# Optimization experiments

Measured on AMD Instinct MI355X. Metric: run time of the kernel, lower is better.

## Reference

```python
import jax, jax.numpy as jnp
import numpy as np

NUM_ENTS = 1000
NUM_RELS = 100
HIDDEN = 200
N_QUERY = 50000
N_HIST = 1000000
ALPHA = 0.5


def setup_inputs() -> dict:
    key = jax.random.key(0)
    ks = jax.random.split(key, 12)
    s = 0.05  # small init for numerical stability (xavier-like scale)
    return {
        "ent_emb": jax.random.normal(ks[0], (NUM_ENTS, HIDDEN), jnp.float32) * s,
        "rel_emb": jax.random.normal(ks[1], (NUM_RELS, HIDDEN), jnp.float32) * s,
        "tim_emb": jax.random.normal(ks[2], (1, HIDDEN), jnp.float32) * s,
        "g_w": jax.random.normal(ks[3], (3 * HIDDEN, HIDDEN), jnp.float32) * s,
        "g_b": jnp.zeros((HIDDEN,), jnp.float32),
        "c_w": jax.random.normal(ks[4], (3 * HIDDEN, HIDDEN), jnp.float32) * s,
        "c_b": jnp.zeros((HIDDEN,), jnp.float32),
        "hist_sub": jax.random.randint(ks[5], (N_HIST,), 0, NUM_ENTS, jnp.int32),
        "hist_rel": jax.random.randint(ks[6], (N_HIST,), 0, NUM_RELS, jnp.int32),
        "hist_obj": jax.random.randint(ks[7], (N_HIST,), 0, NUM_ENTS, jnp.int32),
        "sub": jax.random.randint(ks[8], (N_QUERY,), 0, NUM_ENTS, jnp.int32),
        "rel": jax.random.randint(ks[9], (N_QUERY,), 0, NUM_RELS, jnp.int32),
    }


def reference(ent_emb, rel_emb, tim_emb, g_w, g_b, c_w, c_b,
              hist_sub, hist_rel, hist_obj, sub, rel):
    E = ent_emb.shape[0]
    R = rel_emb.shape[0]
    N = sub.shape[0]
    # Triple-count histogram over all history graphs (fused scatter-add;
    # equivalent to the per-graph python loop vocab[s,r,o] += 1).
    vocab = jnp.zeros((E, R, E), jnp.float32).at[hist_sub, hist_rel, hist_obj].add(1.0)
    # Query features: [N, 3H]
    x = jnp.concatenate(
        [ent_emb[sub], rel_emb[rel], jnp.broadcast_to(tim_emb, (N, tim_emb.shape[1]))],
        axis=1)
    # Generate-mode score distribution
    gscore = jax.nn.softmax(x @ g_w + g_b, axis=1)  # [N, H]
    # Copy-mode mask: 1 where the (sub, rel) pair occurred in history
    mask = (vocab[sub, rel].sum(axis=1, keepdims=True) != 0).astype(x.dtype)  # [N, 1]
    cscore = jax.nn.softmax(jnp.tanh(x @ c_w + c_b) + mask, axis=1)  # [N, H]
    fscore = gscore + ALPHA * (cscore - gscore)
    return jnp.log(fscore)
```

## Files before the change

kernel.cpp:

```cpp
#include <hip/hip_runtime.h>
#include <math.h>

#define HIDDEN 200
#define LOG2E 1.4426950408889634f
#define LN2   0.6931471805599453f

typedef float f32x4 __attribute__((ext_vector_type(4)));

__global__ __launch_bounds__(256) void precompute_kernel(
    const float* __restrict__ ent, const float* __restrict__ rel,
    const float* __restrict__ tim,
    const float* __restrict__ g_w, const float* __restrict__ g_b,
    const float* __restrict__ c_w, const float* __restrict__ c_b,
    float* __restrict__ EA, float* __restrict__ EB) {
  const int mode = blockIdx.y;
  const float* w = mode ? c_w : g_w;
  const float* bias = mode ? c_b : g_b;
  const bool is_ent = blockIdx.x < 500;
  const int row0 = is_ent ? blockIdx.x * 2 : (blockIdx.x - 500) * 2;
  const float* in = is_ent ? ent : rel;
  const int k0 = is_ent ? 0 : 200;
  float* obase = is_ent ? (EA + row0 * 400 + mode * 200)
                        : (EB + row0 * 400 + mode * 200);

  __shared__ float a0[HIDDEN], a1[HIDDEN], tl[HIDDEN];
  const int c = threadIdx.x;
  if (c < HIDDEN) {
    a0[c] = in[row0 * HIDDEN + c];
    a1[c] = in[(row0 + 1) * HIDDEN + c];
    if (!is_ent) tl[c] = tim[c];
  }
  __syncthreads();
  if (c >= HIDDEN) return;

  const float* wp = w + k0 * HIDDEN + c;
  float acc0a = 0.f, acc0b = 0.f, acc1a = 0.f, acc1b = 0.f;
  #pragma unroll 4
  for (int k = 0; k < 100; ++k) {
    float w0 = wp[k * HIDDEN];
    float w1 = wp[(k + 100) * HIDDEN];
    acc0a += a0[k] * w0;
    acc0b += a0[k + 100] * w1;
    acc1a += a1[k] * w0;
    acc1b += a1[k + 100] * w1;
  }
  float r0 = acc0a + acc0b;
  float r1 = acc1a + acc1b;
  if (!is_ent) {
    const float* wt = w + 400 * HIDDEN + c;
    float ta = 0.f, tb = 0.f;
    #pragma unroll 4
    for (int k = 0; k < 100; ++k) {
      ta += tl[k] * wt[k * HIDDEN];
      tb += tl[k + 100] * wt[(k + 100) * HIDDEN];
    }
    float extra = ta + tb + bias[c];
    r0 += extra;
    r1 += extra;
  }
  if (mode == 0) {
    r0 = __builtin_amdgcn_exp2f(r0 * LOG2E);
    r1 = __builtin_amdgcn_exp2f(r1 * LOG2E);
  }
  obase[c] = r0;
  obase[400 + c] = r1;
}

__global__ __launch_bounds__(256) void query_kernel(
    const float* __restrict__ EA, const float* __restrict__ EB,
    const int* __restrict__ sub, const int* __restrict__ rel,
    float* __restrict__ out, int N) {
  int gtid = blockIdx.x * blockDim.x + threadIdx.x;
  int q = gtid >> 6;
  int lane = threadIdx.x & 63;
  if (q >= N) return;

  int s = __builtin_amdgcn_readfirstlane(sub[q]);
  int r = __builtin_amdgcn_readfirstlane(rel[q]);
  bool act = lane < (HIDDEN / 4);

  const f32x4* ea = (const f32x4*)(EA + s * 400);
  const f32x4* eb = (const f32x4*)(EB + r * 400);

  f32x4 eg, ec;
  float sg = 0.f, sc = 0.f;
  if (act) {
    eg = ea[lane] * eb[lane];
    sg = (eg[0] + eg[1]) + (eg[2] + eg[3]);
    f32x4 xc = ea[lane + 50] + eb[lane + 50];
    #pragma unroll
    for (int j = 0; j < 4; ++j) {
      float e2 = __builtin_amdgcn_exp2f(xc[j] * (2.f * LOG2E));
      float th = (e2 - 1.f) * __builtin_amdgcn_rcpf(e2 + 1.f);
      ec[j] = __builtin_amdgcn_exp2f(th * LOG2E);
      sc += ec[j];
    }
  }
  #pragma unroll
  for (int m = 32; m > 0; m >>= 1) {
    sg += __shfl_xor(sg, m);
    sc += __shfl_xor(sc, m);
  }

  if (act) {
    float kl = __builtin_amdgcn_logf(2.f * sg * sc) * LN2;
    f32x4 o;
    #pragma unroll
    for (int j = 0; j < 4; ++j) {
      float num = eg[j] * sc + ec[j] * sg;
      o[j] = fmaf(__builtin_amdgcn_logf(num), LN2, -kl);
    }
    __builtin_nontemporal_store(o, (f32x4*)(out + q * HIDDEN) + lane);
  }
}

extern "C" void kernel_launch(void* const* d_in, const int* in_sizes, int n_in,
                              void* d_out, int out_size, void* d_ws, size_t ws_size,
                              hipStream_t stream) {
  const float* ent  = (const float*)d_in[0];
  const float* relE = (const float*)d_in[1];
  const float* tim  = (const float*)d_in[2];
  const float* g_w  = (const float*)d_in[3];
  const float* g_b  = (const float*)d_in[4];
  const float* c_w  = (const float*)d_in[5];
  const float* c_b  = (const float*)d_in[6];
  const int* sub = (const int*)d_in[10];
  const int* rel = (const int*)d_in[11];
  float* out = (float*)d_out;
  int N = in_sizes[10];

  float* ws = (float*)d_ws;
  float* EA = ws;
  float* EB = ws + 400000;

  dim3 grid1(550, 2);
  precompute_kernel<<<grid1, 256, 0, stream>>>(ent, relE, tim, g_w, g_b, c_w,
                                               c_b, EA, EB);

  long long threads = (long long)N * 64;
  int blocks = (int)((threads + 255) / 256);
  query_kernel<<<blocks, 256, 0, stream>>>(EA, EB, sub, rel, out, N);
}
```

Before: 125.2 us.

## Precompute per (sub,rel) softmax normalizers and drop wave reductions in query kernel

Adds a pair_kernel that computes the gen and copy softmax denominators for all 1000x100 (sub,rel) pairs into workspace tables. The query kernel then reads these sums and maps one thread per float4 output, so it no longer needs a 64-lane wavefront per query, idle lanes, or shuffle reductions. The cost is an extra launch and a sequential 200-step loop per pair, which computes 100k pairs against 50k queries, plus a gather into the SG/SC tables.

New measurement: 141.8 us. 13.2% more time.

```diff
diff --git a/kernel.cpp b/kernel.cpp
--- a/kernel.cpp
+++ b/kernel.cpp
@@ -66,52 +66,61 @@
   obase[400 + c] = r1;
 }
 
+__global__ __launch_bounds__(128) void pair_kernel(
+    const float* __restrict__ EA, const float* __restrict__ EB,
+    float* __restrict__ SG, float* __restrict__ SC) {
+  const int s = blockIdx.x;
+  __shared__ float row[400];
+  for (int i = threadIdx.x; i < 400; i += 128) row[i] = EA[s * 400 + i];
+  __syncthreads();
+  const int r = threadIdx.x;
+  if (r >= 100) return;
+
+  const float* ebg = EB + r * 400;
+  const float* ebc = ebg + 200;
+  float sg = 0.f, sc = 0.f;
+  #pragma unroll 4
+  for (int k = 0; k < 200; ++k) {
+    sg = fmaf(row[k], ebg[k], sg);
+    float x = row[200 + k] + ebc[k];
+    float e2 = __builtin_amdgcn_exp2f(x * (2.f * LOG2E));
+    float th = (e2 - 1.f) * __builtin_amdgcn_rcpf(e2 + 1.f);
+    sc += __builtin_amdgcn_exp2f(th * LOG2E);
+  }
+  SG[s * 100 + r] = sg;
+  SC[s * 100 + r] = sc;
+}
+
 __global__ __launch_bounds__(256) void query_kernel(
     const float* __restrict__ EA, const float* __restrict__ EB,
+    const float* __restrict__ SG, const float* __restrict__ SC,
     const int* __restrict__ sub, const int* __restrict__ rel,
-    float* __restrict__ out, int N) {
-  int gtid = blockIdx.x * blockDim.x + threadIdx.x;
-  int q = gtid >> 6;
-  int lane = threadIdx.x & 63;
-  if (q >= N) return;
+    float* __restrict__ out, int total) {
+  int t = blockIdx.x * blockDim.x + threadIdx.x;
+  if (t >= total) return;
+  unsigned q = (unsigned)t / 50u;
+  unsigned j = (unsigned)t - q * 50u;
 
-  int s = __builtin_amdgcn_readfirstlane(sub[q]);
-  int r = __builtin_amdgcn_readfirstlane(rel[q]);
-  bool act = lane < (HIDDEN / 4);
+  int s = sub[q];
+  int r = rel[q];
+  float isg = 0.5f * __builtin_amdgcn_rcpf(SG[s * 100 + r]);
+  float isc = 0.5f * __builtin_amdgcn_rcpf(SC[s * 100 + r]);
 
   const f32x4* ea = (const f32x4*)(EA + s * 400);
   const f32x4* eb = (const f32x4*)(EB + r * 400);
+  f32x4 eg = ea[j] * eb[j];
+  f32x4 xc = ea[j + 50] + eb[j + 50];
 
-  f32x4 eg, ec;
-  float sg = 0.f, sc = 0.f;
-  if (act) {
-    eg = ea[lane] * eb[lane];
-    sg = (eg[0] + eg[1]) + (eg[2] + eg[3]);
-    f32x4 xc = ea[lane + 50] + eb[lane + 50];
-    #pragma unroll
-    for (int j = 0; j < 4; ++j) {
-      float e2 = __builtin_amdgcn_exp2f(xc[j] * (2.f * LOG2E));
-      float th = (e2 - 1.f) * __builtin_amdgcn_rcpf(e2 + 1.f);
-      ec[j] = __builtin_amdgcn_exp2f(th * LOG2E);
-      sc += ec[j];
-    }
+  f32x4 o;
+  #pragma unroll
+  for (int i = 0; i < 4; ++i) {
+    float e2 = __builtin_amdgcn_exp2f(xc[i] * (2.f * LOG2E));
+    float th = (e2 - 1.f) * __builtin_amdgcn_rcpf(e2 + 1.f);
+    float ec = __builtin_amdgcn_exp2f(th * LOG2E);
+    float v = fmaf(eg[i], isg, ec * isc);
+    o[i] = __builtin_amdgcn_logf(v) * LN2;
   }
-  #pragma unroll
-  for (int m = 32; m > 0; m >>= 1) {
-    sg += __shfl_xor(sg, m);
-    sc += __shfl_xor(sc, m);
-  }
-
-  if (act) {
-    float kl = __builtin_amdgcn_logf(2.f * sg * sc) * LN2;
-    f32x4 o;
-    #pragma unroll
-    for (int j = 0; j < 4; ++j) {
-      float num = eg[j] * sc + ec[j] * sg;
-      o[j] = fmaf(__builtin_amdgcn_logf(num), LN2, -kl);
-    }
-    __builtin_nontemporal_store(o, (f32x4*)(out + q * HIDDEN) + lane);
-  }
+  __builtin_nontemporal_store(o, (f32x4*)out + t);
 }
 
 extern "C" void kernel_launch(void* const* d_in, const int* in_sizes, int n_in,
@@ -132,12 +141,16 @@
   float* ws = (float*)d_ws;
   float* EA = ws;
   float* EB = ws + 400000;
+  float* SG = ws + 440000;
+  float* SC = ws + 540000;
 
   dim3 grid1(550, 2);
   precompute_kernel<<<grid1, 256, 0, stream>>>(ent, relE, tim, g_w, g_b, c_w,
                                                c_b, EA, EB);
+  pair_kernel<<<1000, 128, 0, stream>>>(EA, EB, SG, SC);
 
-  long long threads = (long long)N * 64;
-  int blocks = (int)((threads + 255) / 256);
-  query_kernel<<<blocks, 256, 0, stream>>>(EA, EB, sub, rel, out, N);
+  int total = N * 50;
+  int blocks = (total + 255) / 256;
+  query_kernel<<<blocks, 256, 0, stream>>>(EA, EB, SG, SC, sub, rel, out,
+                                           total);
 }
```

## Fuse precompute and query kernels into one persistent kernel with grid barrier

Applied to the files above, without the earlier changes.

Merges the projection precompute and the per-query softmax/log kernel into a single persistent kernel of 768 blocks. The blocks first stride over the 1100 precompute work items, then meet at a global atomic barrier, then grid-stride over the queries one wave per query. This removes one kernel launch and the gap between the two kernels. In exchange it adds a memset launch, a spin-wait barrier that needs all blocks resident at once, and fewer waves in flight for the query phase.

Result: slower. 207.9 us (+66.1%).

```diff
diff --git a/kernel.cpp b/kernel.cpp
--- a/kernel.cpp
+++ b/kernel.cpp
@@ -4,113 +4,129 @@
 #define HIDDEN 200
 #define LOG2E 1.4426950408889634f
 #define LN2   0.6931471805599453f
+#define NBLK 768
+#define VBLK 1100
 
 typedef float f32x4 __attribute__((ext_vector_type(4)));
 
-__global__ __launch_bounds__(256) void precompute_kernel(
-    const float* __restrict__ ent, const float* __restrict__ rel,
+__global__ __launch_bounds__(256, 4) void fused_kernel(
+    const float* __restrict__ ent, const float* __restrict__ relE,
     const float* __restrict__ tim,
     const float* __restrict__ g_w, const float* __restrict__ g_b,
     const float* __restrict__ c_w, const float* __restrict__ c_b,
-    float* __restrict__ EA, float* __restrict__ EB) {
-  const int mode = blockIdx.y;
-  const float* w = mode ? c_w : g_w;
-  const float* bias = mode ? c_b : g_b;
-  const bool is_ent = blockIdx.x < 500;
-  const int row0 = is_ent ? blockIdx.x * 2 : (blockIdx.x - 500) * 2;
-  const float* in = is_ent ? ent : rel;
-  const int k0 = is_ent ? 0 : 200;
-  float* obase = is_ent ? (EA + row0 * 400 + mode * 200)
-                        : (EB + row0 * 400 + mode * 200);
-
+    const int* __restrict__ sub, const int* __restrict__ rel,
+    float* __restrict__ EA, float* __restrict__ EB,
+    unsigned* __restrict__ bar, float* __restrict__ out, int N) {
   __shared__ float a0[HIDDEN], a1[HIDDEN], tl[HIDDEN];
   const int c = threadIdx.x;
-  if (c < HIDDEN) {
-    a0[c] = in[row0 * HIDDEN + c];
-    a1[c] = in[(row0 + 1) * HIDDEN + c];
-    if (!is_ent) tl[c] = tim[c];
+
+  for (int vb = blockIdx.x; vb < VBLK; vb += NBLK) {
+    const int mode = vb / 550;
+    const int x = vb - mode * 550;
+    const float* w = mode ? c_w : g_w;
+    const float* bias = mode ? c_b : g_b;
+    const bool is_ent = x < 500;
+    const int row0 = is_ent ? x * 2 : (x - 500) * 2;
+    const float* in = is_ent ? ent : relE;
+    const int k0 = is_ent ? 0 : 200;
+    float* obase = (is_ent ? EA : EB) + row0 * 400 + mode * 200;
+
+    if (c < HIDDEN) {
+      a0[c] = in[row0 * HIDDEN + c];
+      a1[c] = in[(row0 + 1) * HIDDEN + c];
+      if (!is_ent) tl[c] = tim[c];
+    }
+    __syncthreads();
+    if (c < HIDDEN) {
+      const float* wp = w + k0 * HIDDEN + c;
+      float acc0a = 0.f, acc0b = 0.f, acc1a = 0.f, acc1b = 0.f;
+      #pragma unroll 4
+      for (int k = 0; k < 100; ++k) {
+        float w0 = wp[k * HIDDEN];
+        float w1 = wp[(k + 100) * HIDDEN];
+        acc0a += a0[k] * w0;
+        acc0b += a0[k + 100] * w1;
+        acc1a += a1[k] * w0;
+        acc1b += a1[k + 100] * w1;
+      }
+      float r0 = acc0a + acc0b;
+      float r1 = acc1a + acc1b;
+      if (!is_ent) {
+        const float* wt = w + 400 * HIDDEN + c;
+        float ta = 0.f, tb = 0.f;
+        #pragma unroll 4
+        for (int k = 0; k < 100; ++k) {
+          ta += tl[k] * wt[k * HIDDEN];
+          tb += tl[k + 100] * wt[(k + 100) * HIDDEN];
+        }
+        float extra = ta + tb + bias[c];
+        r0 += extra;
+        r1 += extra;
+      }
+      if (mode == 0) {
+        r0 = __builtin_amdgcn_exp2f(r0 * LOG2E);
+        r1 = __builtin_amdgcn_exp2f(r1 * LOG2E);
+      }
+      obase[c] = r0;
+      obase[400 + c] = r1;
+    }
+    __syncthreads();
+  }
+
+  __syncthreads();
+  if (threadIdx.x == 0) {
+    __threadfence();
+    if (atomicAdd(&bar[0], 1u) == NBLK - 1u) {
+      __threadfence();
+      atomicExch(&bar[16], 1u);
+    } else {
+      while (__hip_atomic_load(&bar[16], __ATOMIC_RELAXED,
+                               __HIP_MEMORY_SCOPE_AGENT) == 0u)
+        __builtin_amdgcn_s_sleep(8);
+    }
+    __threadfence();
   }
   __syncthreads();
-  if (c >= HIDDEN) return;
 
-  const float* wp = w + k0 * HIDDEN + c;
-  float acc0a = 0.f, acc0b = 0.f, acc1a = 0.f, acc1b = 0.f;
-  #pragma unroll 4
-  for (int k = 0; k < 100; ++k) {
-    float w0 = wp[k * HIDDEN];
-    float w1 = wp[(k + 100) * HIDDEN];
-    acc0a += a0[k] * w0;
-    acc0b += a0[k + 100] * w1;
-    acc1a += a1[k] * w0;
-    acc1b += a1[k + 100] * w1;
-  }
-  float r0 = acc0a + acc0b;
-  float r1 = acc1a + acc1b;
-  if (!is_ent) {
-    const float* wt = w + 400 * HIDDEN + c;
-    float ta = 0.f, tb = 0.f;
-    #pragma unroll 4
-    for (int k = 0; k < 100; ++k) {
-      ta += tl[k] * wt[k * HIDDEN];
-      tb += tl[k + 100] * wt[(k + 100) * HIDDEN];
+  const int lane = threadIdx.x & 63;
+  const bool act = lane < (HIDDEN / 4);
+  const int nwaves = NBLK * 4;
+  const int w0 = blockIdx.x * 4 + (threadIdx.x >> 6);
+  for (int q = w0; q < N; q += nwaves) {
+    int s = __builtin_amdgcn_readfirstlane(sub[q]);
+    int r = __builtin_amdgcn_readfirstlane(rel[q]);
+    const f32x4* ea = (const f32x4*)(EA + s * 400);
+    const f32x4* eb = (const f32x4*)(EB + r * 400);
+
+    f32x4 eg, ec;
+    float sg = 0.f, sc = 0.f;
+    if (act) {
+      eg = ea[lane] * eb[lane];
+      sg = (eg[0] + eg[1]) + (eg[2] + eg[3]);
+      f32x4 xc = ea[lane + 50] + eb[lane + 50];
+      #pragma unroll
+      for (int j = 0; j < 4; ++j) {
+        float e2 = __builtin_amdgcn_exp2f(xc[j] * (2.f * LOG2E));
+        float th = (e2 - 1.f) * __builtin_amdgcn_rcpf(e2 + 1.f);
+        ec[j] = __builtin_amdgcn_exp2f(th * LOG2E);
+        sc += ec[j];
+      }
     }
-    float extra = ta + tb + bias[c];
-    r0 += extra;
-    r1 += extra;
-  }
-  if (mode == 0) {
-    r0 = __builtin_amdgcn_exp2f(r0 * LOG2E);
-    r1 = __builtin_amdgcn_exp2f(r1 * LOG2E);
-  }
-  obase[c] = r0;
-  obase[400 + c] = r1;
-}
-
-__global__ __launch_bounds__(256) void query_kernel(
-    const float* __restrict__ EA, const float* __restrict__ EB,
-    const int* __restrict__ sub, const int* __restrict__ rel,
-    float* __restrict__ out, int N) {
-  int gtid = blockIdx.x * blockDim.x + threadIdx.x;
-  int q = gtid >> 6;
-  int lane = threadIdx.x & 63;
-  if (q >= N) return;
-
-  int s = __builtin_amdgcn_readfirstlane(sub[q]);
-  int r = __builtin_amdgcn_readfirstlane(rel[q]);
-  bool act = lane < (HIDDEN / 4);
-
-  const f32x4* ea = (const f32x4*)(EA + s * 400);
-  const f32x4* eb = (const f32x4*)(EB + r * 400);
-
-  f32x4 eg, ec;
-  float sg = 0.f, sc = 0.f;
-  if (act) {
-    eg = ea[lane] * eb[lane];
-    sg = (eg[0] + eg[1]) + (eg[2] + eg[3]);
-    f32x4 xc = ea[lane + 50] + eb[lane + 50];
     #pragma unroll
-    for (int j = 0; j < 4; ++j) {
-      float e2 = __builtin_amdgcn_exp2f(xc[j] * (2.f * LOG2E));
-      float th = (e2 - 1.f) * __builtin_amdgcn_rcpf(e2 + 1.f);
-      ec[j] = __builtin_amdgcn_exp2f(th * LOG2E);
-      sc += ec[j];
+    for (int m = 32; m > 0; m >>= 1) {
+      sg += __shfl_xor(sg, m);
+      sc += __shfl_xor(sc, m);
     }
-  }
-  #pragma unroll
-  for (int m = 32; m > 0; m >>= 1) {
-    sg += __shfl_xor(sg, m);
-    sc += __shfl_xor(sc, m);
-  }
-
-  if (act) {
-    float kl = __builtin_amdgcn_logf(2.f * sg * sc) * LN2;
-    f32x4 o;
-    #pragma unroll
-    for (int j = 0; j < 4; ++j) {
-      float num = eg[j] * sc + ec[j] * sg;
-      o[j] = fmaf(__builtin_amdgcn_logf(num), LN2, -kl);
+    if (act) {
+      float kl = __builtin_amdgcn_logf(2.f * sg * sc) * LN2;
+      f32x4 o;
+      #pragma unroll
+      for (int j = 0; j < 4; ++j) {
+        float num = eg[j] * sc + ec[j] * sg;
+        o[j] = fmaf(__builtin_amdgcn_logf(num), LN2, -kl);
+      }
+      __builtin_nontemporal_store(o, (f32x4*)(out + q * HIDDEN) + lane);
     }
-    __builtin_nontemporal_store(o, (f32x4*)(out + q * HIDDEN) + lane);
   }
 }
 
@@ -132,12 +148,9 @@
   float* ws = (float*)d_ws;
   float* EA = ws;
   float* EB = ws + 400000;
+  unsigned* bar = (unsigned*)(ws + 448000);
 
-  dim3 grid1(550, 2);
-  precompute_kernel<<<grid1, 256, 0, stream>>>(ent, relE, tim, g_w, g_b, c_w,
-                                               c_b, EA, EB);
-
-  long long threads = (long long)N * 64;
-  int blocks = (int)((threads + 255) / 256);
-  query_kernel<<<blocks, 256, 0, stream>>>(EA, EB, sub, rel, out, N);
+  hipMemsetAsync((void*)bar, 0, 256, stream);
+  fused_kernel<<<NBLK, 256, 0, stream>>>(ent, relE, tim, g_w, g_b, c_w, c_b,
+                                         sub, rel, EA, EB, bar, out, N);
 }
```
